# Optimization experiments

Hardware: AMD Instinct MI355X
Metric: run time of the kernel (lower is better)

Reference implementation:

```python
import jax, jax.numpy as jnp
import numpy as np

LN_EPS = 1e-5


def setup_inputs() -> dict:
    key = jax.random.key(0)
    k1, k2, k3 = jax.random.split(key, 3)
    B, L, D = 4096, 200, 128
    padded_embeddings = jax.random.normal(k1, (B, L, D), dtype=jnp.float32)
    lengths = jnp.maximum(jax.random.randint(k2, (B,), 0, L), 1).astype(jnp.int64)
    w_att = jax.random.normal(k3, (D,), dtype=jnp.float32) * (1.0 / np.sqrt(D))
    b_att = jnp.zeros((1,), dtype=jnp.float32)
    ln_gamma = jnp.ones((D,), dtype=jnp.float32)
    ln_beta = jnp.zeros((D,), dtype=jnp.float32)
    return {
        "padded_embeddings": padded_embeddings,
        "lengths": lengths,
        "w_att": w_att,
        "b_att": b_att,
        "ln_gamma": ln_gamma,
        "ln_beta": ln_beta,
    }


def reference(padded_embeddings, lengths, w_att, b_att, ln_gamma, ln_beta):
    # attention scores: Linear(D, 1) then squeeze -> [B, L]
    scores = jnp.einsum("bld,d->bl", padded_embeddings, w_att) + b_att[0]
    L = padded_embeddings.shape[1]
    mask = jnp.arange(L)[None, :] < lengths[:, None]          # [B, L]
    scores = jnp.where(mask, scores, -jnp.inf)
    attn = jax.nn.softmax(scores, axis=-1)                    # [B, L]
    pooled = jnp.einsum("bld,bl->bd", padded_embeddings, attn)  # [B, D]
    # dropout is identity in eval mode; layernorm over last dim
    mu = jnp.mean(pooled, axis=-1, keepdims=True)
    var = jnp.var(pooled, axis=-1, keepdims=True)
    normed = (pooled - mu) * jax.lax.rsqrt(var + LN_EPS)
    return normed * ln_gamma + ln_beta
```

## Files before the change

### kernel.cpp

```cpp
#include <hip/hip_runtime.h>
#include <cfloat>
#include <cmath>

#define LN_EPS 1e-5f

constexpr int L   = 200;
constexpr int D   = 128;
constexpr int LPW = 50;
constexpr int ITER = 25;

__global__ __launch_bounds__(256)
void fue_kernel(const float* __restrict__ emb,
                const int*   __restrict__ lengths,
                const float* __restrict__ w_att,
                const float* __restrict__ b_att,
                const float* __restrict__ gamma,
                const float* __restrict__ beta,
                float* __restrict__ out) {
    const int b    = blockIdx.x;
    const int tid  = threadIdx.x;
    const int wave = tid >> 6;
    const int lane = tid & 63;
    const int half = lane >> 5;
    const int hl   = lane & 31;

    __shared__ float sc[L];
    __shared__ float red[16];
    __shared__ float partial[4][D];

    const int   len  = lengths[b];
    const float bias = b_att[0];

    const float4 wv = ((const float4*)w_att)[hl];

    const float* row = emb + (size_t)b * (L * D);

    float4 cache[ITER];

    #pragma unroll
    for (int j = 0; j < ITER; ++j) {
        const int l = wave * LPW + 2 * j + half;
        const float4 x = *(const float4*)(row + l * D + hl * 4);
        cache[j] = x;
        float s = x.x * wv.x + x.y * wv.y + x.z * wv.z + x.w * wv.w;
        s += __shfl_xor(s, 1);
        s += __shfl_xor(s, 2);
        s += __shfl_xor(s, 4);
        s += __shfl_xor(s, 8);
        s += __shfl_xor(s, 16);
        if (hl == 0)
            sc[l] = (l < len) ? (s + bias) : -FLT_MAX;
    }
    __syncthreads();

    float v = (tid < L) ? sc[tid] : -FLT_MAX;
    float m = v;
    m = fmaxf(m, __shfl_xor(m, 1));
    m = fmaxf(m, __shfl_xor(m, 2));
    m = fmaxf(m, __shfl_xor(m, 4));
    m = fmaxf(m, __shfl_xor(m, 8));
    m = fmaxf(m, __shfl_xor(m, 16));
    m = fmaxf(m, __shfl_xor(m, 32));
    if (lane == 0) red[wave] = m;
    __syncthreads();
    m = fmaxf(fmaxf(red[0], red[1]), fmaxf(red[2], red[3]));

    float e = (tid < L) ? __expf(v - m) : 0.0f;
    if (tid < L) sc[tid] = e;
    float s = e;
    s += __shfl_xor(s, 1);
    s += __shfl_xor(s, 2);
    s += __shfl_xor(s, 4);
    s += __shfl_xor(s, 8);
    s += __shfl_xor(s, 16);
    s += __shfl_xor(s, 32);
    if (lane == 0) red[4 + wave] = s;
    __syncthreads();
    const float inv = 1.0f / (red[4] + red[5] + red[6] + red[7]);

    float4 acc = make_float4(0.f, 0.f, 0.f, 0.f);
    #pragma unroll
    for (int j = 0; j < ITER; ++j) {
        const int l = wave * LPW + 2 * j + half;
        const float a = sc[l] * inv;
        acc.x += a * cache[j].x;
        acc.y += a * cache[j].y;
        acc.z += a * cache[j].z;
        acc.w += a * cache[j].w;
    }
    acc.x += __shfl_xor(acc.x, 32);
    acc.y += __shfl_xor(acc.y, 32);
    acc.z += __shfl_xor(acc.z, 32);
    acc.w += __shfl_xor(acc.w, 32);
    if (half == 0)
        *(float4*)&partial[wave][hl * 4] = acc;
    __syncthreads();

    float p = 0.f;
    if (tid < D)
        p = partial[0][tid] + partial[1][tid] + partial[2][tid] + partial[3][tid];

    float s1 = p, s2 = p * p;
    s1 += __shfl_xor(s1, 1);  s2 += __shfl_xor(s2, 1);
    s1 += __shfl_xor(s1, 2);  s2 += __shfl_xor(s2, 2);
    s1 += __shfl_xor(s1, 4);  s2 += __shfl_xor(s2, 4);
    s1 += __shfl_xor(s1, 8);  s2 += __shfl_xor(s2, 8);
    s1 += __shfl_xor(s1, 16); s2 += __shfl_xor(s2, 16);
    s1 += __shfl_xor(s1, 32); s2 += __shfl_xor(s2, 32);
    if (lane == 0 && wave < 2) { red[8 + wave] = s1; red[10 + wave] = s2; }
    __syncthreads();

    const float sum1 = red[8] + red[9];
    const float sum2 = red[10] + red[11];
    const float mu   = sum1 * (1.0f / D);
    const float var  = sum2 * (1.0f / D) - mu * mu;
    const float rstd = rsqrtf(var + LN_EPS);

    if (tid < D)
        out[(size_t)b * D + tid] = (p - mu) * rstd * gamma[tid] + beta[tid];
}

extern "C" void kernel_launch(void* const* d_in, const int* in_sizes, int n_in,
                              void* d_out, int out_size, void* d_ws, size_t ws_size,
                              hipStream_t stream) {
    const float* emb     = (const float*)d_in[0];
    const int*   lengths = (const int*)d_in[1];
    const float* w_att   = (const float*)d_in[2];
    const float* b_att   = (const float*)d_in[3];
    const float* gamma   = (const float*)d_in[4];
    const float* beta    = (const float*)d_in[5];
    float* out = (float*)d_out;

    const int B = in_sizes[1];
    fue_kernel<<<B, 256, 0, stream>>>(emb, lengths, w_att, b_att, gamma, beta, out);
}
```

Before: 551.5 us.

## Skip padded rows, stage embeddings in LDS as bf16, widen blocks to 512

Loads only the valid rows of each sequence instead of all 200, skipping memory traffic for padded positions. The loaded rows are rounded to bf16 and stored in shared memory for the pooling pass rather than held in registers. Blocks are enlarged to 16 half-wave row groups with more partial reductions. The bf16 staging reduces the precision of the pooled sum, and the large LDS footprint limits occupancy.

```diff
diff --git a/kernel.cpp b/kernel.cpp
--- a/kernel.cpp
+++ b/kernel.cpp
@@ -4,12 +4,10 @@
 
 #define LN_EPS 1e-5f
 
-constexpr int L   = 200;
-constexpr int D   = 128;
-constexpr int LPW = 50;
-constexpr int ITER = 25;
+constexpr int L = 200;
+constexpr int D = 128;
 
-__global__ __launch_bounds__(256)
+__global__ __launch_bounds__(512, 4)
 void fue_kernel(const float* __restrict__ emb,
                 const int*   __restrict__ lengths,
                 const float* __restrict__ w_att,
@@ -21,39 +19,47 @@
     const int tid  = threadIdx.x;
     const int wave = tid >> 6;
     const int lane = tid & 63;
-    const int half = lane >> 5;
-    const int hl   = lane & 31;
+    const int hw   = tid >> 5;
+    const int hl   = tid & 31;
 
-    __shared__ float sc[L];
+    __shared__ __align__(16) unsigned short row16[L * D];
+    __shared__ float att[L];
+    __shared__ float partial[16][D];
     __shared__ float red[16];
-    __shared__ float partial[4][D];
 
     const int   len  = lengths[b];
     const float bias = b_att[0];
-
-    const float4 wv = ((const float4*)w_att)[hl];
-
+    const float4 wv  = ((const float4*)w_att)[hl];
     const float* row = emb + (size_t)b * (L * D);
 
-    float4 cache[ITER];
+    const int iters = (len + 15) >> 4;
 
-    #pragma unroll
-    for (int j = 0; j < ITER; ++j) {
-        const int l = wave * LPW + 2 * j + half;
-        const float4 x = *(const float4*)(row + l * D + hl * 4);
-        cache[j] = x;
-        float s = x.x * wv.x + x.y * wv.y + x.z * wv.z + x.w * wv.w;
-        s += __shfl_xor(s, 1);
-        s += __shfl_xor(s, 2);
-        s += __shfl_xor(s, 4);
-        s += __shfl_xor(s, 8);
-        s += __shfl_xor(s, 16);
-        if (hl == 0)
-            sc[l] = (l < len) ? (s + bias) : -FLT_MAX;
+    for (int i = 0; i < iters; ++i) {
+        const int l = hw + (i << 4);
+        if (l < len) {
+            const float4 x = *(const float4*)(row + l * D + hl * 4);
+
+            unsigned bx = __float_as_uint(x.x), by = __float_as_uint(x.y);
+            unsigned bz = __float_as_uint(x.z), bw = __float_as_uint(x.w);
+            bx = (bx + 0x7fffu + ((bx >> 16) & 1u)) >> 16;
+            by = (by + 0x7fffu + ((by >> 16) & 1u)) >> 16;
+            bz = (bz + 0x7fffu + ((bz >> 16) & 1u)) >> 16;
+            bw = (bw + 0x7fffu + ((bw >> 16) & 1u)) >> 16;
+            uint2 pk = make_uint2(bx | (by << 16), bz | (bw << 16));
+            *(uint2*)&row16[l * D + hl * 4] = pk;
+
+            float s = x.x * wv.x + x.y * wv.y + x.z * wv.z + x.w * wv.w;
+            s += __shfl_xor(s, 1);
+            s += __shfl_xor(s, 2);
+            s += __shfl_xor(s, 4);
+            s += __shfl_xor(s, 8);
+            s += __shfl_xor(s, 16);
+            if (hl == 0) att[l] = s + bias;
+        }
     }
     __syncthreads();
 
-    float v = (tid < L) ? sc[tid] : -FLT_MAX;
+    float v = (tid < len) ? att[tid] : -FLT_MAX;
     float m = v;
     m = fmaxf(m, __shfl_xor(m, 1));
     m = fmaxf(m, __shfl_xor(m, 2));
@@ -63,10 +69,13 @@
     m = fmaxf(m, __shfl_xor(m, 32));
     if (lane == 0) red[wave] = m;
     __syncthreads();
-    m = fmaxf(fmaxf(red[0], red[1]), fmaxf(red[2], red[3]));
+    m = red[0];
+    #pragma unroll
+    for (int k = 1; k < 8; ++k) m = fmaxf(m, red[k]);
 
-    float e = (tid < L) ? __expf(v - m) : 0.0f;
-    if (tid < L) sc[tid] = e;
+    const float e = (tid < len) ? __expf(v - m) : 0.0f;
+    if (tid < L) att[tid] = e;
+
     float s = e;
     s += __shfl_xor(s, 1);
     s += __shfl_xor(s, 2);
@@ -74,32 +83,37 @@
     s += __shfl_xor(s, 8);
     s += __shfl_xor(s, 16);
     s += __shfl_xor(s, 32);
-    if (lane == 0) red[4 + wave] = s;
+    if (lane == 0) red[8 + wave] = s;
     __syncthreads();
-    const float inv = 1.0f / (red[4] + red[5] + red[6] + red[7]);
+    float tot = red[8];
+    #pragma unroll
+    for (int k = 1; k < 8; ++k) tot += red[8 + k];
+    const float inv = 1.0f / tot;
 
     float4 acc = make_float4(0.f, 0.f, 0.f, 0.f);
-    #pragma unroll
-    for (int j = 0; j < ITER; ++j) {
-        const int l = wave * LPW + 2 * j + half;
-        const float a = sc[l] * inv;
-        acc.x += a * cache[j].x;
-        acc.y += a * cache[j].y;
-        acc.z += a * cache[j].z;
-        acc.w += a * cache[j].w;
+    for (int i = 0; i < iters; ++i) {
+        const int l = hw + (i << 4);
+        if (l < len) {
+            const float a = att[l] * inv;
+            const uint2 pk = *(const uint2*)&row16[l * D + hl * 4];
+            const float x0 = __uint_as_float(pk.x << 16);
+            const float x1 = __uint_as_float(pk.x & 0xffff0000u);
+            const float x2 = __uint_as_float(pk.y << 16);
+            const float x3 = __uint_as_float(pk.y & 0xffff0000u);
+            acc.x += a * x0;
+            acc.y += a * x1;
+            acc.z += a * x2;
+            acc.w += a * x3;
+        }
     }
-    acc.x += __shfl_xor(acc.x, 32);
-    acc.y += __shfl_xor(acc.y, 32);
-    acc.z += __shfl_xor(acc.z, 32);
-    acc.w += __shfl_xor(acc.w, 32);
-    if (half == 0)
-        *(float4*)&partial[wave][hl * 4] = acc;
+    *(float4*)&partial[hw][hl * 4] = acc;
     __syncthreads();
 
     float p = 0.f;
-    if (tid < D)
-        p = partial[0][tid] + partial[1][tid] + partial[2][tid] + partial[3][tid];
-
+    if (tid < D) {
+        #pragma unroll
+        for (int g = 0; g < 16; ++g) p += partial[g][tid];
+    }
     float s1 = p, s2 = p * p;
     s1 += __shfl_xor(s1, 1);  s2 += __shfl_xor(s2, 1);
     s1 += __shfl_xor(s1, 2);  s2 += __shfl_xor(s2, 2);
@@ -107,17 +121,15 @@
     s1 += __shfl_xor(s1, 8);  s2 += __shfl_xor(s2, 8);
     s1 += __shfl_xor(s1, 16); s2 += __shfl_xor(s2, 16);
     s1 += __shfl_xor(s1, 32); s2 += __shfl_xor(s2, 32);
-    if (lane == 0 && wave < 2) { red[8 + wave] = s1; red[10 + wave] = s2; }
+    if (lane == 0 && wave < 2) { red[wave] = s1; red[2 + wave] = s2; }
     __syncthreads();
 
-    const float sum1 = red[8] + red[9];
-    const float sum2 = red[10] + red[11];
-    const float mu   = sum1 * (1.0f / D);
-    const float var  = sum2 * (1.0f / D) - mu * mu;
-    const float rstd = rsqrtf(var + LN_EPS);
-
-    if (tid < D)
+    if (tid < D) {
+        const float mu   = (red[0] + red[1]) * (1.0f / D);
+        const float var  = (red[2] + red[3]) * (1.0f / D) - mu * mu;
+        const float rstd = rsqrtf(var + LN_EPS);
         out[(size_t)b * D + tid] = (p - mu) * rstd * gamma[tid] + beta[tid];
+    }
 }
 
 extern "C" void kernel_launch(void* const* d_in, const int* in_sizes, int n_in,
@@ -132,5 +144,5 @@
     float* out = (float*)d_out;
 
     const int B = in_sizes[1];
-    fue_kernel<<<B, 256, 0, stream>>>(emb, lengths, w_att, b_att, gamma, beta, out);
+    fue_kernel<<<B, 512, 0, stream>>>(emb, lengths, w_att, b_att, gamma, beta, out);
 }
```

Result: faster. 514.0 us (-6.8%).
